# Optimization experiments

Hardware: AMD Instinct MI355X
Metric: run time of the kernel (lower is better)

Reference implementation:

```python
import jax, jax.numpy as jnp
import numpy as np

D = 1024
H = 4
HD = D // H
B = 256
L = 64
DILATIONS = (1, 4, 8, 16)


def setup_inputs() -> dict:
    key = jax.random.key(0)
    ks = jax.random.split(key, 12)
    s = 1.0 / np.sqrt(D)
    return {
        "x": jax.random.normal(ks[0], (B, D), jnp.float32),
        "hist": jax.random.normal(ks[1], (L, B, D), jnp.float32),
        "Wq": jax.random.normal(ks[2], (D, D), jnp.float32) * s,
        "bq": jnp.zeros((D,), jnp.float32),
        "Wk": jax.random.normal(ks[3], (D, D), jnp.float32) * s,
        "bk": jnp.zeros((D,), jnp.float32),
        "Wv": jax.random.normal(ks[4], (D, D), jnp.float32) * s,
        "bv": jnp.zeros((D,), jnp.float32),
        "Wo": jax.random.normal(ks[5], (D, D), jnp.float32) * s,
        "bo": jnp.zeros((D,), jnp.float32),
        "dil_w": jnp.full((len(DILATIONS),), 1.0 / len(DILATIONS), jnp.float32),
        "gamma": jnp.ones((D,), jnp.float32),
        "beta": jnp.zeros((D,), jnp.float32),
    }


def reference(x, hist, Wq, bq, Wk, bk, Wv, bv, Wo, bo, dil_w, gamma, beta):
    scale = 1.0 / np.sqrt(HD)
    q = (x @ Wq + bq).reshape(B, H, HD)  # (B, H, HD)
    attended = []
    for d in DILATIONS:
        # history frames at stride d, concatenated along dim 0 (faithful to torch.cat)
        frames = hist[::d].reshape(-1, D)              # (T', D), T' = ceil(L/d)*B
        k = (frames @ Wk + bk).reshape(-1, H, HD)      # (T', H, HD)
        v = (frames @ Wv + bv).reshape(-1, H, HD)
        s = jnp.einsum('bhd,thd->bht', q, k) * scale   # (B, H, T')
        a = jax.nn.softmax(s, axis=-1)
        attended.append(jnp.einsum('bht,thd->bhd', a, v).reshape(B, D))
    w = jax.nn.softmax(dil_w, axis=0)
    combined = sum(w[i] * attended[i] for i in range(len(DILATIONS)))
    y = x + combined @ Wo + bo
    mu = jnp.mean(y, axis=-1, keepdims=True)
    var = jnp.var(y, axis=-1, keepdims=True)
    return (y - mu) / jnp.sqrt(var + 1e-5) * gamma + beta
```

## Files before the change

### kernel.cpp

```cpp
#include <hip/hip_runtime.h>


#define DD    1024
#define TALL  16384

typedef _Float16 half8  __attribute__((ext_vector_type(8)));
typedef _Float16 half4v __attribute__((ext_vector_type(4)));
typedef float    floatx4 __attribute__((ext_vector_type(4)));
typedef unsigned int u32;

static const size_t OFF_WQT  = 0;
static const size_t OFF_WOT  = 2097152;
static const size_t OFF_WV16 = 4194304;
static const size_t OFF_WK16 = 6291456;
static const size_t OFF_XB   = 8388608;
static const size_t OFF_QS   = 8912896;
static const size_t OFF_G    = 9437184;
static const size_t OFF_WVOT = 11534336;
static const size_t OFF_BVWO = 19922944;
static const size_t OFF_OPP  = 19988480;
static const size_t OFF_PHR  = 24182784;
static const size_t OFF_HB   = 33554432;
static const size_t OFF_PHP  = OFF_HB;
static const size_t OFF_HT   = 67108864;
static const size_t OFF_S    = 100663296;

__device__ __forceinline__ void gl_lds16(const void* g, void* l) {
  __builtin_amdgcn_global_load_lds((const __attribute__((address_space(1))) u32*)g,
                                   (__attribute__((address_space(3))) u32*)l, 16, 0, 0);
}

__global__ void prep_kernel(const float* __restrict__ Wq, const float* __restrict__ Wo,
                            const float* __restrict__ Wv, const float* __restrict__ Wk,
                            const float* __restrict__ hist, const float* __restrict__ x,
                            _Float16* __restrict__ WqT, _Float16* __restrict__ WoT,
                            _Float16* __restrict__ Wv16, _Float16* __restrict__ Wk16,
                            _Float16* __restrict__ histb, _Float16* __restrict__ histT,
                            _Float16* __restrict__ xb) {
  int bid = blockIdx.x, tid = threadIdx.x;
  if (bid < 2048) {
    const float* W = (bid < 1024) ? Wq : Wo;
    _Float16* T = (bid < 1024) ? WqT : WoT;
    int tile = bid & 1023;
    int k0 = (tile & 31) * 32, n0 = (tile >> 5) * 32;
    __shared__ float t32[32][33];
    int tx = tid & 31, ty = tid >> 5;
#pragma unroll
    for (int i = 0; i < 4; i++) {
      int r = ty + i * 8;
      t32[r][tx] = W[(size_t)(k0 + r) * DD + n0 + tx];
    }
    __syncthreads();
#pragma unroll
    for (int i = 0; i < 4; i++) {
      int r = ty + i * 8;
      T[(size_t)(n0 + r) * DD + k0 + tx] = (_Float16)t32[tx][r];
    }
  } else if (bid < 20736) {
    const float* src; _Float16* dst; size_t i;
    if (bid < 3072)       { src = Wv;   dst = Wv16;  i = (size_t)(bid - 2048) * 256 + tid; }
    else if (bid < 4096)  { src = Wk;   dst = Wk16;  i = (size_t)(bid - 3072) * 256 + tid; }
    else if (bid < 20480) { src = hist; dst = histb; i = (size_t)(bid - 4096) * 256 + tid; }
    else                  { src = x;    dst = xb;    i = (size_t)(bid - 20480) * 256 + tid; }
    float4 v = ((const float4*)src)[i];
    half4v h = {(_Float16)v.x, (_Float16)v.y, (_Float16)v.z, (_Float16)v.w};
    *(half4v*)(dst + 4 * i) = h;
  } else {
    int tb = bid - 20736;
    int t0 = (tb & 255) * 64, f0 = (tb >> 8) * 64;
    __shared__ _Float16 lt[64][72];
    int r = tid >> 2, c0 = (tid & 3) * 16;
#pragma unroll
    for (int i = 0; i < 4; i++) {
      float4 v = *(const float4*)&hist[(size_t)(t0 + r) * 1024 + f0 + c0 + i * 4];
      half4v h = {(_Float16)v.x, (_Float16)v.y, (_Float16)v.z, (_Float16)v.w};
      *(half4v*)&lt[r][c0 + i * 4] = h;
    }
    __syncthreads();
    int fr = tid >> 2, tc0 = (tid & 3) * 16;
    half8 o0, o1;
#pragma unroll
    for (int j = 0; j < 8; j++) { o0[j] = lt[tc0 + j][fr]; o1[j] = lt[tc0 + 8 + j][fr]; }
    *(half8*)&histT[(size_t)(f0 + fr) * TALL + t0 + tc0] = o0;
    *(half8*)&histT[(size_t)(f0 + fr) * TALL + t0 + tc0 + 8] = o1;
  }
}

__global__ void bvwo_kernel(const float* __restrict__ bv, const _Float16* __restrict__ WoT,
                            float* __restrict__ bvwo) {
  int j = blockIdx.x * 256 + threadIdx.x;
  const half8* row = (const half8*)(WoT + (size_t)j * 1024);
  float acc = 0.f;
  for (int c = 0; c < 128; c++) {
    half8 w = row[c];
#pragma unroll
    for (int e = 0; e < 8; e++) acc += bv[c * 8 + e] * (float)w[e];
  }
  bvwo[j] = acc;
}

__device__ __forceinline__ void gemm_core(const _Float16* __restrict__ A, size_t lda,
                                          const _Float16* __restrict__ B, size_t ldb,
                                          int kIters, _Float16* As, _Float16* Bs,
                                          int tid, floatx4 acc[4][4]) {
  int lane = tid & 63, w = tid >> 6;
  int l15 = lane & 15, quad = lane >> 4;
  int wm = (w >> 1) * 64, wn = (w & 1) * 64;
  int swz = ((tid & 3) ^ ((tid >> 3) & 3)) * 8;
  int pch = (quad ^ ((l15 >> 1) & 3)) * 8;
  const char* gA0 = (const char*)(A + (size_t)(tid >> 2) * lda + swz);
  const char* gA1 = (const char*)(A + ((size_t)(tid >> 2) + 64) * lda + swz);
  const char* gB0 = (const char*)(B + (size_t)(tid >> 2) * ldb + swz);
  const char* gB1 = (const char*)(B + ((size_t)(tid >> 2) + 64) * ldb + swz);
  _Float16* lA0 = As + w * 512; _Float16* lA1 = As + 2048 + w * 512;
  _Float16* lB0 = Bs + w * 512; _Float16* lB1 = Bs + 2048 + w * 512;
  for (int kk = 0; kk < kIters; kk++) {
    __syncthreads();
    size_t off = (size_t)kk * 64;
    gl_lds16(gA0 + off, lA0);
    gl_lds16(gA1 + off, lA1);
    gl_lds16(gB0 + off, lB0);
    gl_lds16(gB1 + off, lB1);
    __syncthreads();
    half8 a[4];
#pragma unroll
    for (int mi = 0; mi < 4; mi++) a[mi] = *(const half8*)&As[(wm + mi * 16 + l15) * 32 + pch];
#pragma unroll
    for (int ni = 0; ni < 4; ni++) {
      half8 b8 = *(const half8*)&Bs[(wn + ni * 16 + l15) * 32 + pch];
#pragma unroll
      for (int mi = 0; mi < 4; mi++)
        acc[mi][ni] = __builtin_amdgcn_mfma_f32_16x16x32_f16(a[mi], b8, acc[mi][ni], 0, 0, 0);
    }
  }
}

template <bool OUTF32>
__launch_bounds__(256, 3)
__global__ void gemm_f16_kernel(const _Float16* __restrict__ A, size_t lda, size_t aoffz,
                                const _Float16* __restrict__ B, size_t ldb, size_t boffz,
                                int kIters, const float* __restrict__ bias, float scale,
                                void* __restrict__ C, size_t ldc, size_t coffz) {
  __shared__ __align__(16) _Float16 As[4096];
  __shared__ __align__(16) _Float16 Bs[4096];
  int tid = threadIdx.x;
  const _Float16* Ab = A + aoffz * blockIdx.z + (size_t)(blockIdx.y * 128) * lda;
  const _Float16* Bb = B + boffz * blockIdx.z + (size_t)(blockIdx.x * 128) * ldb;
  floatx4 acc[4][4];
  floatx4 zero = {0.f, 0.f, 0.f, 0.f};
#pragma unroll
  for (int a = 0; a < 4; a++)
#pragma unroll
    for (int b = 0; b < 4; b++) acc[a][b] = zero;
  gemm_core(Ab, lda, Bb, ldb, kIters, As, Bs, tid, acc);
  int lane = tid & 63, w = tid >> 6;
  int l15 = lane & 15, quad = lane >> 4;
  int wm = (w >> 1) * 64, wn = (w & 1) * 64;
#pragma unroll
  for (int mi = 0; mi < 4; mi++)
#pragma unroll
    for (int ni = 0; ni < 4; ni++) {
      int colg = blockIdx.x * 128 + wn + ni * 16 + l15;
      float bv = bias ? bias[colg] : 0.f;
#pragma unroll
      for (int r = 0; r < 4; r++) {
        int rowg = blockIdx.y * 128 + wm + mi * 16 + quad * 4 + r;
        float v = (acc[mi][ni][r] + bv) * scale;
        size_t idx = coffz * blockIdx.z + (size_t)rowg * ldc + colg;
        if (OUTF32) ((float*)C)[idx] = v;
        else ((_Float16*)C)[idx] = (_Float16)v;
      }
    }
}

__launch_bounds__(256, 3)
__global__ void gemm_ph_kernel(const _Float16* __restrict__ P, const _Float16* __restrict__ histT,
                               float* __restrict__ part) {
  __shared__ __align__(16) _Float16 As[4096];
  __shared__ __align__(16) _Float16 Bs[4096];
  int tid = threadIdx.x;
  int h = blockIdx.z >> 3, sp = blockIdx.z & 7;
  const _Float16* Ab = P + (size_t)h * 4194304 + (size_t)(blockIdx.y * 128) * TALL + sp * 2048;
  const _Float16* Bb = histT + (size_t)(blockIdx.x * 128) * TALL + sp * 2048;
  floatx4 acc[4][4];
  floatx4 zero = {0.f, 0.f, 0.f, 0.f};
#pragma unroll
  for (int a = 0; a < 4; a++)
#pragma unroll
    for (int b = 0; b < 4; b++) acc[a][b] = zero;
  gemm_core(Ab, TALL, Bb, TALL, 64, As, Bs, tid, acc);
  int lane = tid & 63, w = tid >> 6;
  int l15 = lane & 15, quad = lane >> 4;
  int wm = (w >> 1) * 64, wn = (w & 1) * 64;
#pragma unroll
  for (int mi = 0; mi < 4; mi++)
#pragma unroll
    for (int ni = 0; ni < 4; ni++) {
      int k = blockIdx.x * 128 + wn + ni * 16 + l15;
#pragma unroll
      for (int r = 0; r < 4; r++) {
        int q = blockIdx.y * 128 + wm + mi * 16 + quad * 4 + r;
        part[(size_t)blockIdx.z * 262144 + (size_t)q * 1024 + k] = acc[mi][ni][r];
      }
    }
}

__global__ void reduce_ph_kernel(const float* __restrict__ part, _Float16* __restrict__ PHred) {
  size_t e4 = ((size_t)blockIdx.x * 256 + threadIdx.x) * 4;
  int q = (int)(e4 >> 12);
  int hk = (int)(e4 & 4095);
  int h = hk >> 10, k = hk & 1023;
  float4 s = {0.f, 0.f, 0.f, 0.f};
#pragma unroll
  for (int sp = 0; sp < 8; sp++) {
    float4 p = *(const float4*)&part[(size_t)(h * 8 + sp) * 262144 + (size_t)q * 1024 + k];
    s.x += p.x; s.y += p.y; s.z += p.z; s.w += p.w;
  }
  half4v o = {(_Float16)s.x, (_Float16)s.y, (_Float16)s.z, (_Float16)s.w};
  *(half4v*)&PHred[e4] = o;
}

__global__ void softmax_kernel(_Float16* __restrict__ S, const float* __restrict__ dil_w) {
  int r = blockIdx.x, tid = threadIdx.x;
  _Float16* row = S + (size_t)r * TALL;
  int lane = tid & 63, w = tid >> 6;
  half8 v[8];
  float mloc = -1e30f;
#pragma unroll
  for (int i = 0; i < 8; i++) {
    v[i] = *(const half8*)&row[((size_t)i * 256 + tid) * 8];
#pragma unroll
    for (int j = 0; j < 8; j++) mloc = fmaxf(mloc, (float)v[i][j]);
  }
  __shared__ float wmax[4];
  __shared__ float Zf[64];
  __shared__ float Zd[4];
  __shared__ float cf[64];
#pragma unroll
  for (int off = 1; off <= 32; off <<= 1) mloc = fmaxf(mloc, __shfl_xor(mloc, off, 64));
  if (lane == 0) wmax[w] = mloc;
  __syncthreads();
  float m = fmaxf(fmaxf(wmax[0], wmax[1]), fmaxf(wmax[2], wmax[3]));
  float es[8];
#pragma unroll
  for (int i = 0; i < 8; i++) {
    float s = 0.f;
#pragma unroll
    for (int j = 0; j < 8; j++) s += __expf((float)v[i][j] - m);
#pragma unroll
    for (int off = 1; off <= 16; off <<= 1) s += __shfl_xor(s, off, 64);
    es[i] = s;
  }
  if ((lane & 31) == 0) {
    int half = tid >> 5;
#pragma unroll
    for (int i = 0; i < 8; i++) Zf[i * 8 + half] = es[i];
  }
  __syncthreads();
  if (tid < 4) {
    int step = 1 << (tid + (tid ? 1 : 0));
    float z = 0.f;
    for (int f = 0; f < 64; f += step) z += Zf[f];
    Zd[tid] = z;
  }
  __syncthreads();
  if (tid < 64) {
    float w0 = dil_w[0], w1 = dil_w[1], w2 = dil_w[2], w3 = dil_w[3];
    float wmx = fmaxf(fmaxf(w0, w1), fmaxf(w2, w3));
    float e0 = __expf(w0 - wmx), e1 = __expf(w1 - wmx), e2 = __expf(w2 - wmx), e3 = __expf(w3 - wmx);
    float wsum = e0 + e1 + e2 + e3;
    float c = (e0 / wsum) / Zd[0];
    if ((tid & 3) == 0) c += (e1 / wsum) / Zd[1];
    if ((tid & 7) == 0) c += (e2 / wsum) / Zd[2];
    if ((tid & 15) == 0) c += (e3 / wsum) / Zd[3];
    cf[tid] = c * 256.0f;
  }
  __syncthreads();
#pragma unroll
  for (int i = 0; i < 8; i++) {
    float c = cf[i * 8 + (tid >> 5)];
    half8 o;
#pragma unroll
    for (int j = 0; j < 8; j++) o[j] = (_Float16)(__expf((float)v[i][j] - m) * c);
    *(half8*)&row[((size_t)i * 256 + tid) * 8] = o;
  }
}

__global__ void ln_kernel(const float* __restrict__ x, const float* __restrict__ part2,
                          const float* __restrict__ bo, const float* __restrict__ bvwo,
                          const float* __restrict__ gamma, const float* __restrict__ beta,
                          float* __restrict__ out) {
  int b = blockIdx.x, t = threadIdx.x;
  __shared__ float red[8];
  float y[4];
  float sum = 0.f, sq = 0.f;
#pragma unroll
  for (int i = 0; i < 4; i++) {
    int j = t + i * 256;
    float v = x[(size_t)b * 1024 + j] + bo[j] + bvwo[j];
#pragma unroll
    for (int z = 0; z < 4; z++) v += part2[(size_t)z * 262144 + (size_t)b * 1024 + j];
    y[i] = v;
    sum += v;
    sq += v * v;
  }
#pragma unroll
  for (int off = 1; off < 64; off <<= 1) {
    sum += __shfl_xor(sum, off, 64);
    sq += __shfl_xor(sq, off, 64);
  }
  int w = t >> 6, lane = t & 63;
  if (lane == 0) { red[w] = sum; red[4 + w] = sq; }
  __syncthreads();
  sum = red[0] + red[1] + red[2] + red[3];
  sq = red[4] + red[5] + red[6] + red[7];
  float mu = sum * (1.f / 1024.f);
  float var = sq * (1.f / 1024.f) - mu * mu;
  float inv = rsqrtf(var + 1e-5f);
#pragma unroll
  for (int i = 0; i < 4; i++) {
    int j = t + i * 256;
    out[(size_t)b * 1024 + j] = (y[i] - mu) * inv * gamma[j] + beta[j];
  }
}

extern "C" void kernel_launch(void* const* d_in, const int* in_sizes, int n_in,
                              void* d_out, int out_size, void* d_ws, size_t ws_size,
                              hipStream_t stream) {
  const float* x     = (const float*)d_in[0];
  const float* hist  = (const float*)d_in[1];
  const float* Wq    = (const float*)d_in[2];
  const float* bq    = (const float*)d_in[3];
  const float* Wk    = (const float*)d_in[4];
  const float* Wv    = (const float*)d_in[6];
  const float* bv    = (const float*)d_in[7];
  const float* Wo    = (const float*)d_in[8];
  const float* bo    = (const float*)d_in[9];
  const float* dil_w = (const float*)d_in[10];
  const float* gamma = (const float*)d_in[11];
  const float* beta  = (const float*)d_in[12];
  char* ws = (char*)d_ws;

  _Float16* WqT   = (_Float16*)(ws + OFF_WQT);
  _Float16* WoT   = (_Float16*)(ws + OFF_WOT);
  _Float16* Wv16  = (_Float16*)(ws + OFF_WV16);
  _Float16* Wk16  = (_Float16*)(ws + OFF_WK16);
  _Float16* xb    = (_Float16*)(ws + OFF_XB);
  _Float16* Qs    = (_Float16*)(ws + OFF_QS);
  _Float16* G     = (_Float16*)(ws + OFF_G);
  _Float16* WVOT  = (_Float16*)(ws + OFF_WVOT);
  float* bvwo     = (float*)(ws + OFF_BVWO);
  float* oppart   = (float*)(ws + OFF_OPP);
  _Float16* PHred = (_Float16*)(ws + OFF_PHR);
  _Float16* histb = (_Float16*)(ws + OFF_HB);
  float* phpart   = (float*)(ws + OFF_PHP);
  _Float16* histT = (_Float16*)(ws + OFF_HT);
  _Float16* Sb    = (_Float16*)(ws + OFF_S);

  prep_kernel<<<dim3(24832), 256, 0, stream>>>(Wq, Wo, Wv, Wk, hist, x,
                                               WqT, WoT, Wv16, Wk16, histb, histT, xb);
  bvwo_kernel<<<dim3(4), 256, 0, stream>>>(bv, WoT, bvwo);
  gemm_f16_kernel<false><<<dim3(8, 8, 4), 256, 0, stream>>>(
      WoT, 1024, 256, Wv16, 1024, 256, 8, nullptr, 1.0f, (void*)WVOT, 4096, 1024);
  gemm_f16_kernel<false><<<dim3(8, 2, 1), 256, 0, stream>>>(
      xb, 1024, 0, WqT, 1024, 0, 32, bq, 0.0625f, (void*)Qs, 1024, 0);
  gemm_f16_kernel<false><<<dim3(8, 2, 4), 256, 0, stream>>>(
      Qs, 1024, 256, Wk16, 1024, 256, 8, nullptr, 1.0f, (void*)G, 1024, 262144);
  gemm_f16_kernel<false><<<dim3(128, 2, 4), 256, 0, stream>>>(
      G, 1024, 262144, histb, 1024, 0, 32, nullptr, 1.0f, (void*)Sb, TALL, 4194304);
  softmax_kernel<<<dim3(1024), 256, 0, stream>>>(Sb, dil_w);
  gemm_ph_kernel<<<dim3(8, 2, 32), 256, 0, stream>>>(Sb, histT, phpart);
  reduce_ph_kernel<<<dim3(1024), 256, 0, stream>>>(phpart, PHred);
  gemm_f16_kernel<true><<<dim3(8, 2, 4), 256, 0, stream>>>(
      PHred, 4096, 1024, WVOT, 4096, 1024, 32, nullptr, 1.0f / 256.0f,
      (void*)oppart, 1024, 262144);
  ln_kernel<<<dim3(256), 256, 0, stream>>>(x, oppart, bo, bvwo, gamma, beta, (float*)d_out);
}
```

Measured before the change: 360.4 us.

## Fold Wq·Wkᵀ per head, fuse hist conversions, merge weight packs, drop softmax max

Per-head Wq·Wkᵀ products (scaled, with the folded bq bias) are precomputed so G comes from one x@WQKT GEMM, replacing the separate Q and G GEMMs. The hist fp16 copy and the transposed copy are now written in one prep pass, so hist is read once instead of twice. The WoᵀWv and WqWkᵀ packing GEMMs and the bias projections run in one combined launch. The S and PH GEMMs get a remapped 1-D grid for L2 locality, and the output GEMM uses 8-way split-K. Softmax no longer subtracts the row max and caches the exponentials, which saves a pass but can overflow if the logits are large.

```diff
diff --git a/kernel.cpp b/kernel.cpp
--- a/kernel.cpp
+++ b/kernel.cpp
@@ -9,73 +9,76 @@
 typedef float    floatx4 __attribute__((ext_vector_type(4)));
 typedef unsigned int u32;
 
-static const size_t OFF_WQT  = 0;
-static const size_t OFF_WOT  = 2097152;
-static const size_t OFF_WV16 = 4194304;
-static const size_t OFF_WK16 = 6291456;
+static const size_t OFF_WOT  = 0;
+static const size_t OFF_WV16 = 2097152;
+static const size_t OFF_WK16 = 4194304;
+static const size_t OFF_WQ16 = 6291456;
 static const size_t OFF_XB   = 8388608;
-static const size_t OFF_QS   = 8912896;
-static const size_t OFF_G    = 9437184;
-static const size_t OFF_WVOT = 11534336;
-static const size_t OFF_BVWO = 19922944;
-static const size_t OFF_OPP  = 19988480;
-static const size_t OFF_PHR  = 24182784;
-static const size_t OFF_HB   = 33554432;
+static const size_t OFF_G    = 8912896;
+static const size_t OFF_WVOT = 11010048;
+static const size_t OFF_WQKT = 19398656;
+static const size_t OFF_BVWO = 27787264;
+static const size_t OFF_BQK  = 27791360;
+static const size_t OFF_PHR  = 27807744;
+static const size_t OFF_OPP  = 29904896;
+static const size_t OFF_HB   = 38293504;
 static const size_t OFF_PHP  = OFF_HB;
-static const size_t OFF_HT   = 67108864;
-static const size_t OFF_S    = 100663296;
+static const size_t OFF_HT   = 71848960;
+static const size_t OFF_S    = 105403392;
 
 __device__ __forceinline__ void gl_lds16(const void* g, void* l) {
   __builtin_amdgcn_global_load_lds((const __attribute__((address_space(1))) u32*)g,
                                    (__attribute__((address_space(3))) u32*)l, 16, 0, 0);
 }
 
-__global__ void prep_kernel(const float* __restrict__ Wq, const float* __restrict__ Wo,
-                            const float* __restrict__ Wv, const float* __restrict__ Wk,
-                            const float* __restrict__ hist, const float* __restrict__ x,
-                            _Float16* __restrict__ WqT, _Float16* __restrict__ WoT,
-                            _Float16* __restrict__ Wv16, _Float16* __restrict__ Wk16,
-                            _Float16* __restrict__ histb, _Float16* __restrict__ histT,
-                            _Float16* __restrict__ xb) {
+__global__ void prep_kernel(const float* __restrict__ Wo, const float* __restrict__ Wv,
+                            const float* __restrict__ Wk, const float* __restrict__ Wq,
+                            const float* __restrict__ x, const float* __restrict__ hist,
+                            _Float16* __restrict__ WoT, _Float16* __restrict__ Wv16,
+                            _Float16* __restrict__ Wk16, _Float16* __restrict__ Wq16,
+                            _Float16* __restrict__ xb, _Float16* __restrict__ histb,
+                            _Float16* __restrict__ histT) {
   int bid = blockIdx.x, tid = threadIdx.x;
-  if (bid < 2048) {
-    const float* W = (bid < 1024) ? Wq : Wo;
-    _Float16* T = (bid < 1024) ? WqT : WoT;
-    int tile = bid & 1023;
-    int k0 = (tile & 31) * 32, n0 = (tile >> 5) * 32;
+  if (bid < 1024) {
+    int k0 = (bid & 31) * 32, n0 = (bid >> 5) * 32;
     __shared__ float t32[32][33];
     int tx = tid & 31, ty = tid >> 5;
 #pragma unroll
     for (int i = 0; i < 4; i++) {
       int r = ty + i * 8;
-      t32[r][tx] = W[(size_t)(k0 + r) * DD + n0 + tx];
+      t32[r][tx] = Wo[(size_t)(k0 + r) * DD + n0 + tx];
     }
     __syncthreads();
 #pragma unroll
     for (int i = 0; i < 4; i++) {
       int r = ty + i * 8;
-      T[(size_t)(n0 + r) * DD + k0 + tx] = (_Float16)t32[tx][r];
-    }
-  } else if (bid < 20736) {
+      WoT[(size_t)(n0 + r) * DD + k0 + tx] = (_Float16)t32[tx][r];
+    }
+  } else if (bid < 4352) {
     const float* src; _Float16* dst; size_t i;
-    if (bid < 3072)       { src = Wv;   dst = Wv16;  i = (size_t)(bid - 2048) * 256 + tid; }
-    else if (bid < 4096)  { src = Wk;   dst = Wk16;  i = (size_t)(bid - 3072) * 256 + tid; }
-    else if (bid < 20480) { src = hist; dst = histb; i = (size_t)(bid - 4096) * 256 + tid; }
-    else                  { src = x;    dst = xb;    i = (size_t)(bid - 20480) * 256 + tid; }
+    if (bid < 2048)      { src = Wv; dst = Wv16; i = (size_t)(bid - 1024) * 256 + tid; }
+    else if (bid < 3072) { src = Wk; dst = Wk16; i = (size_t)(bid - 2048) * 256 + tid; }
+    else if (bid < 4096) { src = Wq; dst = Wq16; i = (size_t)(bid - 3072) * 256 + tid; }
+    else                 { src = x;  dst = xb;   i = (size_t)(bid - 4096) * 256 + tid; }
     float4 v = ((const float4*)src)[i];
     half4v h = {(_Float16)v.x, (_Float16)v.y, (_Float16)v.z, (_Float16)v.w};
     *(half4v*)(dst + 4 * i) = h;
   } else {
-    int tb = bid - 20736;
+    int tb = bid - 4352;
     int t0 = (tb & 255) * 64, f0 = (tb >> 8) * 64;
     __shared__ _Float16 lt[64][72];
     int r = tid >> 2, c0 = (tid & 3) * 16;
+    half8 s0, s1;
 #pragma unroll
     for (int i = 0; i < 4; i++) {
       float4 v = *(const float4*)&hist[(size_t)(t0 + r) * 1024 + f0 + c0 + i * 4];
       half4v h = {(_Float16)v.x, (_Float16)v.y, (_Float16)v.z, (_Float16)v.w};
       *(half4v*)&lt[r][c0 + i * 4] = h;
-    }
+      if (i < 2) { s0[i*4]=h[0]; s0[i*4+1]=h[1]; s0[i*4+2]=h[2]; s0[i*4+3]=h[3]; }
+      else { s1[(i-2)*4]=h[0]; s1[(i-2)*4+1]=h[1]; s1[(i-2)*4+2]=h[2]; s1[(i-2)*4+3]=h[3]; }
+    }
+    *(half8*)&histb[(size_t)(t0 + r) * 1024 + f0 + c0] = s0;
+    *(half8*)&histb[(size_t)(t0 + r) * 1024 + f0 + c0 + 8] = s1;
     __syncthreads();
     int fr = tid >> 2, tc0 = (tid & 3) * 16;
     half8 o0, o1;
@@ -84,19 +87,6 @@
     *(half8*)&histT[(size_t)(f0 + fr) * TALL + t0 + tc0] = o0;
     *(half8*)&histT[(size_t)(f0 + fr) * TALL + t0 + tc0 + 8] = o1;
   }
-}
-
-__global__ void bvwo_kernel(const float* __restrict__ bv, const _Float16* __restrict__ WoT,
-                            float* __restrict__ bvwo) {
-  int j = blockIdx.x * 256 + threadIdx.x;
-  const half8* row = (const half8*)(WoT + (size_t)j * 1024);
-  float acc = 0.f;
-  for (int c = 0; c < 128; c++) {
-    half8 w = row[c];
-#pragma unroll
-    for (int e = 0; e < 8; e++) acc += bv[c * 8 + e] * (float)w[e];
-  }
-  bvwo[j] = acc;
 }
 
 __device__ __forceinline__ void gemm_core(const _Float16* __restrict__ A, size_t lda,
@@ -139,8 +129,8 @@
 __launch_bounds__(256, 3)
 __global__ void gemm_f16_kernel(const _Float16* __restrict__ A, size_t lda, size_t aoffz,
                                 const _Float16* __restrict__ B, size_t ldb, size_t boffz,
-                                int kIters, const float* __restrict__ bias, float scale,
-                                void* __restrict__ C, size_t ldc, size_t coffz) {
+                                int kIters, const float* __restrict__ bias, size_t biasoffz,
+                                float scale, void* __restrict__ C, size_t ldc, size_t coffz) {
   __shared__ __align__(16) _Float16 As[4096];
   __shared__ __align__(16) _Float16 Bs[4096];
   int tid = threadIdx.x;
@@ -161,7 +151,7 @@
 #pragma unroll
     for (int ni = 0; ni < 4; ni++) {
       int colg = blockIdx.x * 128 + wn + ni * 16 + l15;
-      float bv = bias ? bias[colg] : 0.f;
+      float bv = bias ? bias[biasoffz * blockIdx.z + colg] : 0.f;
 #pragma unroll
       for (int r = 0; r < 4; r++) {
         int rowg = blockIdx.y * 128 + wm + mi * 16 + quad * 4 + r;
@@ -174,21 +164,86 @@
 }
 
 __launch_bounds__(256, 3)
-__global__ void gemm_ph_kernel(const _Float16* __restrict__ P, const _Float16* __restrict__ histT,
-                               float* __restrict__ part) {
+__global__ void wpack_kernel(const _Float16* __restrict__ WoT, const _Float16* __restrict__ Wv16,
+                             const _Float16* __restrict__ Wk16, const _Float16* __restrict__ Wq16,
+                             const float* __restrict__ bv, const float* __restrict__ bq,
+                             _Float16* __restrict__ WVOT, _Float16* __restrict__ WQKT,
+                             float* __restrict__ bvwo, float* __restrict__ bqk) {
   __shared__ __align__(16) _Float16 As[4096];
   __shared__ __align__(16) _Float16 Bs[4096];
-  int tid = threadIdx.x;
-  int h = blockIdx.z >> 3, sp = blockIdx.z & 7;
-  const _Float16* Ab = P + (size_t)h * 4194304 + (size_t)(blockIdx.y * 128) * TALL + sp * 2048;
-  const _Float16* Bb = histT + (size_t)(blockIdx.x * 128) * TALL + sp * 2048;
+  int bid = blockIdx.x, tid = threadIdx.x;
+  if (bid < 512) {
+    bool isQK = bid >= 256;
+    int g = bid & 255;
+    int x = g & 7, y = (g >> 3) & 7, z = g >> 6;
+    const _Float16* A = isQK ? Wk16 : WoT;
+    const _Float16* B = isQK ? Wq16 : Wv16;
+    const _Float16* Ab = A + 256 * z + (size_t)(y * 128) * 1024;
+    const _Float16* Bb = B + 256 * z + (size_t)(x * 128) * 1024;
+    floatx4 acc[4][4];
+    floatx4 zero = {0.f, 0.f, 0.f, 0.f};
+#pragma unroll
+    for (int a = 0; a < 4; a++)
+#pragma unroll
+      for (int b = 0; b < 4; b++) acc[a][b] = zero;
+    gemm_core(Ab, 1024, Bb, 1024, 8, As, Bs, tid, acc);
+    float scale = isQK ? 0.0625f : 1.0f;
+    _Float16* C = isQK ? WQKT : WVOT;
+    size_t ldc = isQK ? 1024 : 4096;
+    size_t zoff = isQK ? (size_t)1048576 * z : (size_t)1024 * z;
+    int lane = tid & 63, w = tid >> 6;
+    int l15 = lane & 15, quad = lane >> 4;
+    int wm = (w >> 1) * 64, wn = (w & 1) * 64;
+#pragma unroll
+    for (int mi = 0; mi < 4; mi++)
+#pragma unroll
+      for (int ni = 0; ni < 4; ni++) {
+        int col = x * 128 + wn + ni * 16 + l15;
+#pragma unroll
+        for (int r = 0; r < 4; r++) {
+          int row = y * 128 + wm + mi * 16 + quad * 4 + r;
+          C[zoff + (size_t)row * ldc + col] = (_Float16)(acc[mi][ni][r] * scale);
+        }
+      }
+  } else if (bid < 516) {
+    int j = (bid - 512) * 256 + tid;
+    const half8* row = (const half8*)(WoT + (size_t)j * 1024);
+    float a = 0.f;
+    for (int c = 0; c < 128; c++) {
+      half8 w8 = row[c];
+#pragma unroll
+      for (int e = 0; e < 8; e++) a += bv[c * 8 + e] * (float)w8[e];
+    }
+    bvwo[j] = a;
+  } else {
+    int idx = (bid - 516) * 256 + tid;
+    int h = idx >> 10, f = idx & 1023;
+    const _Float16* row = Wk16 + (size_t)f * 1024 + h * 256;
+    float a = 0.f;
+    for (int n = 0; n < 256; n++) a += bq[h * 256 + n] * (float)row[n];
+    bqk[idx] = a * 0.0625f;
+  }
+}
+
+__launch_bounds__(256, 3)
+__global__ void gemm_s_kernel(const _Float16* __restrict__ G, const _Float16* __restrict__ histb,
+                              _Float16* __restrict__ S) {
+  __shared__ __align__(16) _Float16 As[4096];
+  __shared__ __align__(16) _Float16 Bs[4096];
+  int bid = blockIdx.x, tid = threadIdx.x;
+  int b7 = bid & 7, rr = bid >> 3;
+  int x = ((rr & 15) << 3) | b7;
+  int yh = rr >> 4;
+  int y = yh & 1, h = yh >> 1;
+  const _Float16* Ab = G + (size_t)h * 262144 + (size_t)(y * 128) * 1024;
+  const _Float16* Bb = histb + (size_t)(x * 128) * 1024;
   floatx4 acc[4][4];
   floatx4 zero = {0.f, 0.f, 0.f, 0.f};
 #pragma unroll
   for (int a = 0; a < 4; a++)
 #pragma unroll
     for (int b = 0; b < 4; b++) acc[a][b] = zero;
-  gemm_core(Ab, TALL, Bb, TALL, 64, As, Bs, tid, acc);
+  gemm_core(Ab, 1024, Bb, 1024, 32, As, Bs, tid, acc);
   int lane = tid & 63, w = tid >> 6;
   int l15 = lane & 15, quad = lane >> 4;
   int wm = (w >> 1) * 64, wn = (w & 1) * 64;
@@ -196,57 +251,30 @@
   for (int mi = 0; mi < 4; mi++)
 #pragma unroll
     for (int ni = 0; ni < 4; ni++) {
-      int k = blockIdx.x * 128 + wn + ni * 16 + l15;
+      int col = x * 128 + wn + ni * 16 + l15;
 #pragma unroll
       for (int r = 0; r < 4; r++) {
-        int q = blockIdx.y * 128 + wm + mi * 16 + quad * 4 + r;
-        part[(size_t)blockIdx.z * 262144 + (size_t)q * 1024 + k] = acc[mi][ni][r];
+        int row = y * 128 + wm + mi * 16 + quad * 4 + r;
+        S[(size_t)h * 4194304 + (size_t)row * TALL + col] = (_Float16)acc[mi][ni][r];
       }
     }
-}
-
-__global__ void reduce_ph_kernel(const float* __restrict__ part, _Float16* __restrict__ PHred) {
-  size_t e4 = ((size_t)blockIdx.x * 256 + threadIdx.x) * 4;
-  int q = (int)(e4 >> 12);
-  int hk = (int)(e4 & 4095);
-  int h = hk >> 10, k = hk & 1023;
-  float4 s = {0.f, 0.f, 0.f, 0.f};
-#pragma unroll
-  for (int sp = 0; sp < 8; sp++) {
-    float4 p = *(const float4*)&part[(size_t)(h * 8 + sp) * 262144 + (size_t)q * 1024 + k];
-    s.x += p.x; s.y += p.y; s.z += p.z; s.w += p.w;
-  }
-  half4v o = {(_Float16)s.x, (_Float16)s.y, (_Float16)s.z, (_Float16)s.w};
-  *(half4v*)&PHred[e4] = o;
 }
 
 __global__ void softmax_kernel(_Float16* __restrict__ S, const float* __restrict__ dil_w) {
   int r = blockIdx.x, tid = threadIdx.x;
   _Float16* row = S + (size_t)r * TALL;
-  int lane = tid & 63, w = tid >> 6;
-  half8 v[8];
-  float mloc = -1e30f;
-#pragma unroll
-  for (int i = 0; i < 8; i++) {
-    v[i] = *(const half8*)&row[((size_t)i * 256 + tid) * 8];
-#pragma unroll
-    for (int j = 0; j < 8; j++) mloc = fmaxf(mloc, (float)v[i][j]);
-  }
-  __shared__ float wmax[4];
+  int lane = tid & 63;
+  float ef[8][8];
+  float es[8];
   __shared__ float Zf[64];
   __shared__ float Zd[4];
   __shared__ float cf[64];
 #pragma unroll
-  for (int off = 1; off <= 32; off <<= 1) mloc = fmaxf(mloc, __shfl_xor(mloc, off, 64));
-  if (lane == 0) wmax[w] = mloc;
-  __syncthreads();
-  float m = fmaxf(fmaxf(wmax[0], wmax[1]), fmaxf(wmax[2], wmax[3]));
-  float es[8];
-#pragma unroll
   for (int i = 0; i < 8; i++) {
+    half8 v = *(const half8*)&row[((size_t)i * 256 + tid) * 8];
     float s = 0.f;
 #pragma unroll
-    for (int j = 0; j < 8; j++) s += __expf((float)v[i][j] - m);
+    for (int j = 0; j < 8; j++) { float e = __expf((float)v[j]); ef[i][j] = e; s += e; }
 #pragma unroll
     for (int off = 1; off <= 16; off <<= 1) s += __shfl_xor(s, off, 64);
     es[i] = s;
@@ -281,9 +309,58 @@
     float c = cf[i * 8 + (tid >> 5)];
     half8 o;
 #pragma unroll
-    for (int j = 0; j < 8; j++) o[j] = (_Float16)(__expf((float)v[i][j] - m) * c);
+    for (int j = 0; j < 8; j++) o[j] = (_Float16)(ef[i][j] * c);
     *(half8*)&row[((size_t)i * 256 + tid) * 8] = o;
   }
+}
+
+__launch_bounds__(256, 3)
+__global__ void gemm_ph_kernel(const _Float16* __restrict__ P, const _Float16* __restrict__ histT,
+                               float* __restrict__ part) {
+  __shared__ __align__(16) _Float16 As[4096];
+  __shared__ __align__(16) _Float16 Bs[4096];
+  int bid = blockIdx.x, tid = threadIdx.x;
+  int sp = bid & 7, rr = bid >> 3;
+  int x = rr & 7, yh = rr >> 3;
+  int y = yh & 1, h = yh >> 1;
+  const _Float16* Ab = P + (size_t)h * 4194304 + (size_t)(y * 128) * TALL + sp * 2048;
+  const _Float16* Bb = histT + (size_t)(x * 128) * TALL + sp * 2048;
+  floatx4 acc[4][4];
+  floatx4 zero = {0.f, 0.f, 0.f, 0.f};
+#pragma unroll
+  for (int a = 0; a < 4; a++)
+#pragma unroll
+    for (int b = 0; b < 4; b++) acc[a][b] = zero;
+  gemm_core(Ab, TALL, Bb, TALL, 64, As, Bs, tid, acc);
+  int lane = tid & 63, w = tid >> 6;
+  int l15 = lane & 15, quad = lane >> 4;
+  int wm = (w >> 1) * 64, wn = (w & 1) * 64;
+#pragma unroll
+  for (int mi = 0; mi < 4; mi++)
+#pragma unroll
+    for (int ni = 0; ni < 4; ni++) {
+      int k = x * 128 + wn + ni * 16 + l15;
+#pragma unroll
+      for (int r = 0; r < 4; r++) {
+        int q = y * 128 + wm + mi * 16 + quad * 4 + r;
+        part[(size_t)(h * 8 + sp) * 262144 + (size_t)q * 1024 + k] = acc[mi][ni][r];
+      }
+    }
+}
+
+__global__ void reduce_ph_kernel(const float* __restrict__ part, _Float16* __restrict__ PHred) {
+  size_t e4 = ((size_t)blockIdx.x * 256 + threadIdx.x) * 4;
+  int q = (int)(e4 >> 12);
+  int hk = (int)(e4 & 4095);
+  int h = hk >> 10, k = hk & 1023;
+  float4 s = {0.f, 0.f, 0.f, 0.f};
+#pragma unroll
+  for (int sp = 0; sp < 8; sp++) {
+    float4 p = *(const float4*)&part[(size_t)(h * 8 + sp) * 262144 + (size_t)q * 1024 + k];
+    s.x += p.x; s.y += p.y; s.z += p.z; s.w += p.w;
+  }
+  half4v o = {(_Float16)s.x, (_Float16)s.y, (_Float16)s.z, (_Float16)s.w};
+  *(half4v*)&PHred[e4] = o;
 }
 
 __global__ void ln_kernel(const float* __restrict__ x, const float* __restrict__ part2,
@@ -299,7 +376,7 @@
     int j = t + i * 256;
     float v = x[(size_t)b * 1024 + j] + bo[j] + bvwo[j];
 #pragma unroll
-    for (int z = 0; z < 4; z++) v += part2[(size_t)z * 262144 + (size_t)b * 1024 + j];
+    for (int z = 0; z < 8; z++) v += part2[(size_t)z * 262144 + (size_t)b * 1024 + j];
     y[i] = v;
     sum += v;
     sq += v * v;
@@ -341,38 +418,35 @@
   const float* beta  = (const float*)d_in[12];
   char* ws = (char*)d_ws;
 
-  _Float16* WqT   = (_Float16*)(ws + OFF_WQT);
   _Float16* WoT   = (_Float16*)(ws + OFF_WOT);
   _Float16* Wv16  = (_Float16*)(ws + OFF_WV16);
   _Float16* Wk16  = (_Float16*)(ws + OFF_WK16);
+  _Float16* Wq16  = (_Float16*)(ws + OFF_WQ16);
   _Float16* xb    = (_Float16*)(ws + OFF_XB);
-  _Float16* Qs    = (_Float16*)(ws + OFF_QS);
   _Float16* G     = (_Float16*)(ws + OFF_G);
   _Float16* WVOT  = (_Float16*)(ws + OFF_WVOT);
+  _Float16* WQKT  = (_Float16*)(ws + OFF_WQKT);
   float* bvwo     = (float*)(ws + OFF_BVWO);
+  float* bqk      = (float*)(ws + OFF_BQK);
+  _Float16* PHred = (_Float16*)(ws + OFF_PHR);
   float* oppart   = (float*)(ws + OFF_OPP);
-  _Float16* PHred = (_Float16*)(ws + OFF_PHR);
   _Float16* histb = (_Float16*)(ws + OFF_HB);
   float* phpart   = (float*)(ws + OFF_PHP);
   _Float16* histT = (_Float16*)(ws + OFF_HT);
   _Float16* Sb    = (_Float16*)(ws + OFF_S);
 
-  prep_kernel<<<dim3(24832), 256, 0, stream>>>(Wq, Wo, Wv, Wk, hist, x,
-                                               WqT, WoT, Wv16, Wk16, histb, histT, xb);
-  bvwo_kernel<<<dim3(4), 256, 0, stream>>>(bv, WoT, bvwo);
-  gemm_f16_kernel<false><<<dim3(8, 8, 4), 256, 0, stream>>>(
-      WoT, 1024, 256, Wv16, 1024, 256, 8, nullptr, 1.0f, (void*)WVOT, 4096, 1024);
-  gemm_f16_kernel<false><<<dim3(8, 2, 1), 256, 0, stream>>>(
-      xb, 1024, 0, WqT, 1024, 0, 32, bq, 0.0625f, (void*)Qs, 1024, 0);
+  prep_kernel<<<dim3(8448), 256, 0, stream>>>(Wo, Wv, Wk, Wq, x, hist,
+                                              WoT, Wv16, Wk16, Wq16, xb, histb, histT);
+  wpack_kernel<<<dim3(532), 256, 0, stream>>>(WoT, Wv16, Wk16, Wq16, bv, bq,
+                                              WVOT, WQKT, bvwo, bqk);
   gemm_f16_kernel<false><<<dim3(8, 2, 4), 256, 0, stream>>>(
-      Qs, 1024, 256, Wk16, 1024, 256, 8, nullptr, 1.0f, (void*)G, 1024, 262144);
-  gemm_f16_kernel<false><<<dim3(128, 2, 4), 256, 0, stream>>>(
-      G, 1024, 262144, histb, 1024, 0, 32, nullptr, 1.0f, (void*)Sb, TALL, 4194304);
+      xb, 1024, 0, WQKT, 1024, 1048576, 32, bqk, 1024, 1.0f, (void*)G, 1024, 262144);
+  gemm_s_kernel<<<dim3(1024), 256, 0, stream>>>(G, histb, Sb);
   softmax_kernel<<<dim3(1024), 256, 0, stream>>>(Sb, dil_w);
-  gemm_ph_kernel<<<dim3(8, 2, 32), 256, 0, stream>>>(Sb, histT, phpart);
+  gemm_ph_kernel<<<dim3(512), 256, 0, stream>>>(Sb, histT, phpart);
   reduce_ph_kernel<<<dim3(1024), 256, 0, stream>>>(phpart, PHred);
-  gemm_f16_kernel<true><<<dim3(8, 2, 4), 256, 0, stream>>>(
-      PHred, 4096, 1024, WVOT, 4096, 1024, 32, nullptr, 1.0f / 256.0f,
+  gemm_f16_kernel<true><<<dim3(8, 2, 8), 256, 0, stream>>>(
+      PHred, 4096, 512, WVOT, 4096, 512, 16, nullptr, 0, 1.0f / 256.0f,
       (void*)oppart, 1024, 262144);
   ln_kernel<<<dim3(256), 256, 0, stream>>>(x, oppart, bo, bvwo, gamma, beta, (float*)d_out);
 }
```

New measurement: 320.4 us. 1.12x faster.
